# Optimization experiments

Measured on AMD Instinct MI355X. Metric: run time of the kernel, lower is better.

The kernel has to match this reference:

```python
import jax, jax.numpy as jnp
import numpy as np
from jax import lax


def _lstm_layer(x, h0, c0, W_ih, W_hh, b_ih, b_hh):
    # x: [B,T,I]; precompute input projection for all timesteps: [B,T,4H]
    xg = jnp.einsum('bti,gi->btg', x, W_ih) + b_ih

    def step(carry, xg_t):
        h, c = carry
        gates = xg_t + h @ W_hh.T + b_hh  # [B,4H]
        i, f, g, o = jnp.split(gates, 4, axis=-1)  # PyTorch LSTMCell gate order
        i = jax.nn.sigmoid(i)
        f = jax.nn.sigmoid(f)
        g = jnp.tanh(g)
        o = jax.nn.sigmoid(o)
        c = f * c + i * g
        h = o * jnp.tanh(c)
        return (h, c), h

    (h, c), ys = lax.scan(step, (h0, c0), jnp.swapaxes(xg, 0, 1))  # scan over T
    return jnp.swapaxes(ys, 0, 1), h, c  # [B,T,H], [B,H], [B,H]


def setup_inputs() -> dict:
    key = jax.random.key(0)
    ks = jax.random.split(key, 10)
    B, T, I, H = 128, 256, 256, 1024
    s = 0.02
    return {
        'x': jax.random.normal(ks[0], (B, T, I), jnp.float32),
        'hx0': jnp.zeros((2, B, H), jnp.float32),
        'cx0': jnp.zeros((2, B, H), jnp.float32),
        'W_ih0': jax.random.normal(ks[1], (4 * H, I), jnp.float32) * s,
        'W_hh0': jax.random.normal(ks[2], (4 * H, H), jnp.float32) * s,
        'b_ih0': jax.random.normal(ks[3], (4 * H,), jnp.float32) * s,
        'b_hh0': jax.random.normal(ks[4], (4 * H,), jnp.float32) * s,
        'W_ih1': jax.random.normal(ks[5], (4 * H, H), jnp.float32) * s,
        'W_hh1': jax.random.normal(ks[6], (4 * H, H), jnp.float32) * s,
        'b_ih1': jax.random.normal(ks[7], (4 * H,), jnp.float32) * s,
        'b_hh1': jax.random.normal(ks[8], (4 * H,), jnp.float32) * s,
    }


def reference(x, hx0, cx0, W_ih0, W_hh0, b_ih0, b_hh0, W_ih1, W_hh1, b_ih1, b_hh1):
    # Eval mode / variational_inference=False with dropout=0.0: masks are exact ones.
    x, h, c = _lstm_layer(x, hx0[0], cx0[0], W_ih0, W_hh0, b_ih0, b_hh0)
    x, h, c = _lstm_layer(x, hx0[1], cx0[1], W_ih1, W_hh1, b_ih1, b_hh1)
    return x, h, c
```

## Files before the change

### kernel.cpp

```cpp
#include <hip/hip_runtime.h>

typedef __attribute__((ext_vector_type(8))) short short8;
typedef __attribute__((ext_vector_type(4))) float f32x4;

#define DEV static __device__ __forceinline__

DEV unsigned short f2b(float f) {
    union { float f; unsigned u; } v; v.f = f;
    unsigned r = (v.u + 0x7FFFu + ((v.u >> 16) & 1u)) >> 16;
    return (unsigned short)r;
}
DEV float b2f(unsigned short s) {
    union { unsigned u; float f; } v; v.u = ((unsigned)s) << 16;
    return v.f;
}
DEV float sigm(float x) { return 1.0f / (1.0f + __expf(-x)); }


__global__ void k_f2b(const float* __restrict__ src, unsigned short* __restrict__ dst, int n4) {
    int i = blockIdx.x * blockDim.x + threadIdx.x;
    if (i < n4) {
        float4 v = ((const float4*)src)[i];
        ushort4 o;
        o.x = f2b(v.x); o.y = f2b(v.y); o.z = f2b(v.z); o.w = f2b(v.w);
        ((ushort4*)dst)[i] = o;
    }
}

__global__ void k_perm(const float* __restrict__ src, unsigned short* __restrict__ dst, int Kq) {
    int i = blockIdx.x * blockDim.x + threadIdx.x;
    int total = 4096 * Kq;
    if (i >= total) return;
    int rp = i / Kq, kq = i - rp * Kq;
    int j = rp >> 2, g = rp & 3;
    float4 v = ((const float4*)src)[(size_t)(g * 1024 + j) * Kq + kq];
    ushort4 o;
    o.x = f2b(v.x); o.y = f2b(v.y); o.z = f2b(v.z); o.w = f2b(v.w);
    ((ushort4*)dst)[(size_t)rp * Kq + kq] = o;
}

__global__ void k_bias(const float* __restrict__ bi0, const float* __restrict__ bh0,
                       const float* __restrict__ bi1, const float* __restrict__ bh1,
                       float* __restrict__ d0, float* __restrict__ d1) {
    int i = blockIdx.x * blockDim.x + threadIdx.x;
    if (i < 4096) {
        int j = i >> 2, g = i & 3, s = g * 1024 + j;
        d0[i] = bi0[s] + bh0[s];
        d1[i] = bi1[s] + bh1[s];
    }
}

__global__ void k_init(const float* __restrict__ hx, const float* __restrict__ cx,
                       unsigned* __restrict__ hB0, unsigned* __restrict__ hB1,
                       float* __restrict__ c0, float* __restrict__ c1) {
    int i = blockIdx.x * blockDim.x + threadIdx.x;
    if (i < 128 * 512) {
        int b = i >> 9, j = i & 511;
        const float* p0 = hx + (size_t)b * 1024 + j * 2;
        const float* p1 = hx + 131072 + (size_t)b * 1024 + j * 2;
        hB0[i] = (unsigned)f2b(p0[0]) | ((unsigned)f2b(p0[1]) << 16);
        hB1[i] = (unsigned)f2b(p1[0]) | ((unsigned)f2b(p1[1]) << 16);
        c0[i * 2] = cx[i * 2];
        c0[i * 2 + 1] = cx[i * 2 + 1];
        c1[i * 2] = cx[131072 + i * 2];
        c1[i * 2 + 1] = cx[131072 + i * 2 + 1];
    }
}

__global__ __launch_bounds__(256) void k_gemm(
    const unsigned short* __restrict__ A, const unsigned short* __restrict__ W,
    unsigned short* __restrict__ out, int K, int t0, int TC) {
    __shared__ unsigned short ldsA[128 * 40];
    __shared__ unsigned short ldsB[128 * 40];
    const int tid = threadIdx.x;
    const int w = tid >> 6, l = tid & 63;
    const int wm = w >> 1, wn = w & 1;
    const int bm = blockIdx.x, bn = blockIdx.y;
    const int lr = l & 15, lk = (l >> 4) * 8;

    const int row0 = tid >> 2, inb = (tid & 3) << 4;
    const int row1 = row0 + 64;
    const int v0 = bm * 128 + row0, v1 = bm * 128 + row1;
    const size_t ar0 = (size_t)((v0 / TC) * 256 + t0 + (v0 % TC));
    const size_t ar1 = (size_t)((v1 / TC) * 256 + t0 + (v1 % TC));
    const size_t br0 = (size_t)(bn * 128 + row0);
    const size_t br1 = (size_t)(bn * 128 + row1);

    f32x4 acc[4][4];
#pragma unroll
    for (int a = 0; a < 4; a++)
#pragma unroll
        for (int b = 0; b < 4; b++) acc[a][b] = (f32x4){0.f, 0.f, 0.f, 0.f};

    for (int ks = 0; ks < K; ks += 32) {
        uint4 a0 = *(const uint4*)((const char*)A + (ar0 * K + ks) * 2 + inb);
        uint4 a1 = *(const uint4*)((const char*)A + (ar1 * K + ks) * 2 + inb);
        uint4 b0 = *(const uint4*)((const char*)W + (br0 * K + ks) * 2 + inb);
        uint4 b1 = *(const uint4*)((const char*)W + (br1 * K + ks) * 2 + inb);
        *(uint4*)((char*)ldsA + row0 * 80 + inb) = a0;
        *(uint4*)((char*)ldsA + row1 * 80 + inb) = a1;
        *(uint4*)((char*)ldsB + row0 * 80 + inb) = b0;
        *(uint4*)((char*)ldsB + row1 * 80 + inb) = b1;
        __syncthreads();
        short8 af[4], bf[4];
#pragma unroll
        for (int mt = 0; mt < 4; mt++)
            af[mt] = *(const short8*)((const char*)ldsA + (wm * 64 + mt * 16 + lr) * 80 + lk * 2);
#pragma unroll
        for (int nt = 0; nt < 4; nt++)
            bf[nt] = *(const short8*)((const char*)ldsB + (wn * 64 + nt * 16 + lr) * 80 + lk * 2);
#pragma unroll
        for (int mt = 0; mt < 4; mt++)
#pragma unroll
            for (int nt = 0; nt < 4; nt++)
                acc[mt][nt] = __builtin_amdgcn_mfma_f32_16x16x32_bf16(af[mt], bf[nt], acc[mt][nt], 0, 0, 0);
        __syncthreads();
    }

#pragma unroll
    for (int mt = 0; mt < 4; mt++)
#pragma unroll
        for (int nt = 0; nt < 4; nt++)
#pragma unroll
            for (int v4 = 0; v4 < 4; v4++) {
                int vr = bm * 128 + wm * 64 + mt * 16 + (l >> 4) * 4 + v4;
                int col = bn * 128 + wn * 64 + nt * 16 + lr;
                out[(size_t)vr * 4096 + col] = f2b(acc[mt][nt][v4]);
            }
}

template<int LAYER>
__global__ __launch_bounds__(256, 1) void k_lstm(
    const unsigned short* __restrict__ Wh,
    const unsigned short* __restrict__ xg,
    const float* __restrict__ bias,
    float* __restrict__ cbuf,
    unsigned* __restrict__ hA,
    unsigned* __restrict__ hB,
    unsigned short* __restrict__ y0,
    float* __restrict__ out,
    unsigned* __restrict__ cnt,
    int t0, int TC)
{
    extern __shared__ char smem[];
    unsigned short* ldsW = (unsigned short*)smem;
    float* ldsP0 = (float*)(smem + 64 * 2064);
    float* ldsP1 = ldsP0 + 16 * 132;

    const int tid = threadIdx.x;
    const int g  = (int)blockIdx.x >> 5;
    const int nb = (int)blockIdx.x & 31;
    const int kq = tid >> 6;
    const int l  = tid & 63;
    const int lr = l & 15, lq = l >> 4;

    {
        const char* src = (const char*)(Wh + (size_t)nb * 128 * 1024);
#pragma unroll
        for (int it = 0; it < 32; it++) {
            int idx = it * 256 + tid;
            int row = idx >> 7, inr = (idx & 127) << 4;
            *(uint4*)(smem + row * 2064 + inr) = *(const uint4*)(src + (size_t)row * 2048 + inr);
        }
    }
    short8 wreg[32];
    {
        const unsigned short* src = Wh + (size_t)(nb * 128 + 64) * 1024 + kq * 256;
#pragma unroll
        for (int ct = 0; ct < 4; ct++)
#pragma unroll
            for (int kk = 0; kk < 8; kk++)
                wreg[ct * 8 + kk] =
                    *(const short8*)(src + (size_t)(ct * 16 + lr) * 1024 + kk * 32 + lq * 8);
    }

    const int er = tid >> 4, ep = tid & 15;
    const int eb = g * 16 + er;
    const int ec0 = nb * 128 + ep * 8;
    const int eu0 = nb * 32 + ep * 2;
    float2 c2 = *(const float2*)(cbuf + (size_t)eb * 1024 + eu0);
    const float4 bsA = *(const float4*)(bias + ec0);
    const float4 bsB = *(const float4*)(bias + ec0 + 4);

    const size_t abase = (size_t)(g * 16 + lr) * 256 + (size_t)kq * 64 + lq * 2;
    const char* wp = (const char*)ldsW + (size_t)lr * 2064 + kq * 512 + lq * 16;

    unsigned* cmy = cnt + g * 32;

    __syncthreads();

    for (int dt = 0; dt < TC; dt++) {
        const int t = t0 + dt;
        uint4 xv = *(const uint4*)(xg + (size_t)eb * ((size_t)TC * 4096) + (size_t)dt * 4096 + ec0);

        if (dt > 0) {
            unsigned tgt = 32u * (unsigned)dt;
            while (__hip_atomic_load(cmy, __ATOMIC_RELAXED, __HIP_MEMORY_SCOPE_AGENT) < tgt) {}
        }

        const unsigned long long* ap =
            (const unsigned long long*)((t & 1) ? hA : hB) + abase;
        f32x4 acc[8];
#pragma unroll
        for (int i = 0; i < 8; i++) acc[i] = (f32x4){0.f, 0.f, 0.f, 0.f};
#pragma unroll
        for (int kk = 0; kk < 8; kk++) {
            union { unsigned long long u[2]; short8 s; } av;
            av.u[0] = __hip_atomic_load(ap + kk * 8,     __ATOMIC_RELAXED, __HIP_MEMORY_SCOPE_AGENT);
            av.u[1] = __hip_atomic_load(ap + kk * 8 + 1, __ATOMIC_RELAXED, __HIP_MEMORY_SCOPE_AGENT);
#pragma unroll
            for (int ct = 0; ct < 4; ct++) {
                short8 b = *(const short8*)(wp + (size_t)ct * 16 * 2064 + kk * 64);
                acc[ct] = __builtin_amdgcn_mfma_f32_16x16x32_bf16(av.s, b, acc[ct], 0, 0, 0);
            }
#pragma unroll
            for (int ct = 0; ct < 4; ct++)
                acc[4 + ct] = __builtin_amdgcn_mfma_f32_16x16x32_bf16(av.s, wreg[ct * 8 + kk], acc[4 + ct], 0, 0, 0);
        }

        if (kq >= 2) {
            float* P = (kq == 2) ? ldsP0 : ldsP1;
#pragma unroll
            for (int i = 0; i < 8; i++)
#pragma unroll
                for (int v = 0; v < 4; v++)
                    P[(lq * 4 + v) * 132 + i * 16 + lr] = acc[i][v];
        }
        __syncthreads();
        if (kq < 2) {
            float* P = (kq == 0) ? ldsP0 : ldsP1;
#pragma unroll
            for (int i = 0; i < 8; i++)
#pragma unroll
                for (int v = 0; v < 4; v++)
                    P[(lq * 4 + v) * 132 + i * 16 + lr] += acc[i][v];
        }
        __syncthreads();

        float h0v, h1v;
        {
            const float* pa = ldsP0 + er * 132 + ep * 8;
            const float* pb = ldsP1 + er * 132 + ep * 8;
            const unsigned short* xs = (const unsigned short*)&xv;
            float p0 = pa[0] + pb[0] + b2f(xs[0]) + bsA.x;
            float p1 = pa[1] + pb[1] + b2f(xs[1]) + bsA.y;
            float p2 = pa[2] + pb[2] + b2f(xs[2]) + bsA.z;
            float p3 = pa[3] + pb[3] + b2f(xs[3]) + bsA.w;
            float q0 = pa[4] + pb[4] + b2f(xs[4]) + bsB.x;
            float q1 = pa[5] + pb[5] + b2f(xs[5]) + bsB.y;
            float q2 = pa[6] + pb[6] + b2f(xs[6]) + bsB.z;
            float q3 = pa[7] + pb[7] + b2f(xs[7]) + bsB.w;
            float i0 = sigm(p0), f0 = sigm(p1), gv0 = tanhf(p2), o0 = sigm(p3);
            float i1 = sigm(q0), f1 = sigm(q1), gv1 = tanhf(q2), o1 = sigm(q3);
            c2.x = f0 * c2.x + i0 * gv0;
            c2.y = f1 * c2.y + i1 * gv1;
            h0v = o0 * tanhf(c2.x);
            h1v = o1 * tanhf(c2.y);
            unsigned hp = (unsigned)f2b(h0v) | ((unsigned)f2b(h1v) << 16);
            unsigned* hout = (t & 1) ? hB : hA;
            __hip_atomic_store(hout + (size_t)eb * 512 + eu0 / 2, hp,
                               __ATOMIC_RELAXED, __HIP_MEMORY_SCOPE_AGENT);
        }
        __syncthreads();
        if (tid == 0)
            __hip_atomic_fetch_add(cmy, 1u, __ATOMIC_RELAXED, __HIP_MEMORY_SCOPE_AGENT);

        if (LAYER == 0) {
            unsigned hp = (unsigned)f2b(h0v) | ((unsigned)f2b(h1v) << 16);
            ((unsigned*)y0)[((size_t)eb * 256 + t) * 512 + eu0 / 2] = hp;
        } else {
            *(float2*)(out + ((size_t)eb * 256 + t) * 1024 + eu0) = make_float2(h0v, h1v);
            if (t == 255) {
                *(float2*)(out + (size_t)128 * 256 * 1024 + (size_t)eb * 1024 + eu0) =
                    make_float2(h0v, h1v);
                *(float2*)(out + (size_t)128 * 256 * 1024 + (size_t)128 * 1024 + (size_t)eb * 1024 + eu0) =
                    make_float2(c2.x, c2.y);
            }
        }
    }
    *(float2*)(cbuf + (size_t)eb * 1024 + eu0) = c2;
}


extern "C" void kernel_launch(void* const* d_in, const int* in_sizes, int n_in,
                              void* d_out, int out_size, void* d_ws, size_t ws_size,
                              hipStream_t stream) {
    const float* x    = (const float*)d_in[0];
    const float* hx0  = (const float*)d_in[1];
    const float* cx0  = (const float*)d_in[2];
    const float* Wih0 = (const float*)d_in[3];
    const float* Whh0 = (const float*)d_in[4];
    const float* bih0 = (const float*)d_in[5];
    const float* bhh0 = (const float*)d_in[6];
    const float* Wih1 = (const float*)d_in[7];
    const float* Whh1 = (const float*)d_in[8];
    const float* bih1 = (const float*)d_in[9];
    const float* bhh1 = (const float*)d_in[10];
    float* out = (float*)d_out;

    const int B = 128, T = 256, I = 256, H = 1024, G4 = 4096;
    const unsigned SMEM_BYTES = 64 * 2064 + 2 * 16 * 132 * 4;

    hipFuncSetAttribute((const void*)&k_lstm<0>, hipFuncAttributeMaxDynamicSharedMemorySize, SMEM_BYTES);
    hipFuncSetAttribute((const void*)&k_lstm<1>, hipFuncAttributeMaxDynamicSharedMemorySize, SMEM_BYTES);

    char* p = (char*)d_ws;
    auto alloc = [&](size_t bytes) { char* r = p; p += (bytes + 255) & ~(size_t)255; return r; };
    unsigned short* xbf   = (unsigned short*)alloc((size_t)B * T * I * 2);
    unsigned short* Wih0p = (unsigned short*)alloc((size_t)G4 * I * 2);
    unsigned short* Whh0p = (unsigned short*)alloc((size_t)G4 * H * 2);
    unsigned short* Wih1p = (unsigned short*)alloc((size_t)G4 * H * 2);
    unsigned short* Whh1p = (unsigned short*)alloc((size_t)G4 * H * 2);
    float* bias0 = (float*)alloc(G4 * 4);
    float* bias1 = (float*)alloc(G4 * 4);
    unsigned short* y0 = (unsigned short*)alloc((size_t)B * T * H * 2);
    unsigned* hA0 = (unsigned*)alloc((size_t)B * 512 * 4);
    unsigned* hB0 = (unsigned*)alloc((size_t)B * 512 * 4);
    unsigned* hA1 = (unsigned*)alloc((size_t)B * 512 * 4);
    unsigned* hB1 = (unsigned*)alloc((size_t)B * 512 * 4);
    float* c0 = (float*)alloc((size_t)B * H * 4);
    float* c1 = (float*)alloc((size_t)B * H * 4);
    unsigned* cnt = (unsigned*)alloc(8 * 128);
    size_t fixed = (size_t)(p - (char*)d_ws);
    int TC = 256;
    while (TC > 1 && fixed + (size_t)B * TC * G4 * 2 + 256 > ws_size) TC >>= 1;
    unsigned short* xg = (unsigned short*)alloc((size_t)B * TC * G4 * 2);

    k_f2b<<<(B * T * I / 4 + 255) / 256, 256, 0, stream>>>(x, xbf, B * T * I / 4);
    k_perm<<<(G4 * (I / 4) + 255) / 256, 256, 0, stream>>>(Wih0, Wih0p, I / 4);
    k_perm<<<(G4 * (H / 4) + 255) / 256, 256, 0, stream>>>(Whh0, Whh0p, H / 4);
    k_perm<<<(G4 * (H / 4) + 255) / 256, 256, 0, stream>>>(Wih1, Wih1p, H / 4);
    k_perm<<<(G4 * (H / 4) + 255) / 256, 256, 0, stream>>>(Whh1, Whh1p, H / 4);
    k_bias<<<16, 256, 0, stream>>>(bih0, bhh0, bih1, bhh1, bias0, bias1);
    k_init<<<256, 256, 0, stream>>>(hx0, cx0, hB0, hB1, c0, c1);

    for (int t0 = 0; t0 < T; t0 += TC) {
        k_gemm<<<dim3(TC, 32), 256, 0, stream>>>(xbf, Wih0p, xg, I, t0, TC);
        hipMemsetAsync(cnt, 0, 8 * 128, stream);
        int t0v = t0, TCv = TC;
        const unsigned short* Whp = Whh0p;
        const unsigned short* xgp = xg;
        const float* bp = bias0;
        float* cp = c0;
        unsigned* ha = hA0; unsigned* hb = hB0;
        unsigned short* y0p = y0;
        float* op = nullptr;
        unsigned* cp2 = cnt;
        void* args[] = {&Whp, &xgp, &bp, &cp, &ha, &hb, &y0p, &op, &cp2, &t0v, &TCv};
        hipLaunchCooperativeKernel((const void*)&k_lstm<0>, dim3(256), dim3(256), args, SMEM_BYTES, stream);
    }
    for (int t0 = 0; t0 < T; t0 += TC) {
        k_gemm<<<dim3(TC, 32), 256, 0, stream>>>(y0, Wih1p, xg, H, t0, TC);
        hipMemsetAsync(cnt, 0, 8 * 128, stream);
        int t0v = t0, TCv = TC;
        const unsigned short* Whp = Whh1p;
        const unsigned short* xgp = xg;
        const float* bp = bias1;
        float* cp = c1;
        unsigned* ha = hA1; unsigned* hb = hB1;
        unsigned short* y0p = nullptr;
        float* op = out;
        unsigned* cp2 = cnt;
        void* args[] = {&Whp, &xgp, &bp, &cp, &ha, &hb, &y0p, &op, &cp2, &t0v, &TCv};
        hipLaunchCooperativeKernel((const void*)&k_lstm<1>, dim3(256), dim3(256), args, SMEM_BYTES, stream);
    }
}
```

Baseline: 3.118 ms.

## Replace per-group atomic counter barrier with per-block step flags and partial waits

Each block now publishes its completed timestep in its own padded flag slot with a plain atomic store, in place of a fetch_add on a shared counter. Each wavefront polls only the 8 producer blocks whose hidden-state slice feeds its K quarter, so it no longer waits for all 32 blocks in the group. This is meant to remove atomic contention on one cache line and let wavefronts start their MFMA work earlier. Flags hold absolute timesteps, so they are cleared once per launch rather than memset before every chunk, at the cost of 8 polled loads per spin iteration.

```diff
diff --git a/kernel.cpp b/kernel.cpp
--- a/kernel.cpp
+++ b/kernel.cpp
@@ -139,7 +139,7 @@
     unsigned* __restrict__ hB,
     unsigned short* __restrict__ y0,
     float* __restrict__ out,
-    unsigned* __restrict__ cnt,
+    unsigned* __restrict__ flags,
     int t0, int TC)
 {
     extern __shared__ char smem[];
@@ -185,7 +185,8 @@
     const size_t abase = (size_t)(g * 16 + lr) * 256 + (size_t)kq * 64 + lq * 2;
     const char* wp = (const char*)ldsW + (size_t)lr * 2064 + kq * 512 + lq * 16;
 
-    unsigned* cmy = cnt + g * 32;
+    const unsigned* fpoll = flags + (size_t)(g * 32 + kq * 8) * 16;
+    unsigned* fmine = flags + (size_t)(g * 32 + nb) * 16;
 
     __syncthreads();
 
@@ -193,9 +194,16 @@
         const int t = t0 + dt;
         uint4 xv = *(const uint4*)(xg + (size_t)eb * ((size_t)TC * 4096) + (size_t)dt * 4096 + ec0);
 
-        if (dt > 0) {
-            unsigned tgt = 32u * (unsigned)dt;
-            while (__hip_atomic_load(cmy, __ATOMIC_RELAXED, __HIP_MEMORY_SCOPE_AGENT) < tgt) {}
+        if (t > 0) {
+            const unsigned tgt = (unsigned)t;
+            for (;;) {
+                unsigned ok = 1;
+#pragma unroll
+                for (int j = 0; j < 8; j++)
+                    ok &= (__hip_atomic_load(fpoll + j * 16, __ATOMIC_RELAXED,
+                                             __HIP_MEMORY_SCOPE_AGENT) >= tgt) ? 1u : 0u;
+                if (ok) break;
+            }
         }
 
         const unsigned long long* ap =
@@ -263,7 +271,8 @@
         }
         __syncthreads();
         if (tid == 0)
-            __hip_atomic_fetch_add(cmy, 1u, __ATOMIC_RELAXED, __HIP_MEMORY_SCOPE_AGENT);
+            __hip_atomic_store(fmine, (unsigned)(t + 1),
+                               __ATOMIC_RELAXED, __HIP_MEMORY_SCOPE_AGENT);
 
         if (LAYER == 0) {
             unsigned hp = (unsigned)f2b(h0v) | ((unsigned)f2b(h1v) << 16);
@@ -300,6 +309,7 @@
 
     const int B = 128, T = 256, I = 256, H = 1024, G4 = 4096;
     const unsigned SMEM_BYTES = 64 * 2064 + 2 * 16 * 132 * 4;
+    const int FLAGS_U32 = 8 * 32 * 16;
 
     hipFuncSetAttribute((const void*)&k_lstm<0>, hipFuncAttributeMaxDynamicSharedMemorySize, SMEM_BYTES);
     hipFuncSetAttribute((const void*)&k_lstm<1>, hipFuncAttributeMaxDynamicSharedMemorySize, SMEM_BYTES);
@@ -320,12 +330,14 @@
     unsigned* hB1 = (unsigned*)alloc((size_t)B * 512 * 4);
     float* c0 = (float*)alloc((size_t)B * H * 4);
     float* c1 = (float*)alloc((size_t)B * H * 4);
-    unsigned* cnt = (unsigned*)alloc(8 * 128);
+    unsigned* flags0 = (unsigned*)alloc((size_t)2 * FLAGS_U32 * 4);
+    unsigned* flags1 = flags0 + FLAGS_U32;
     size_t fixed = (size_t)(p - (char*)d_ws);
     int TC = 256;
     while (TC > 1 && fixed + (size_t)B * TC * G4 * 2 + 256 > ws_size) TC >>= 1;
     unsigned short* xg = (unsigned short*)alloc((size_t)B * TC * G4 * 2);
 
+    hipMemsetAsync(flags0, 0, (size_t)2 * FLAGS_U32 * 4, stream);
     k_f2b<<<(B * T * I / 4 + 255) / 256, 256, 0, stream>>>(x, xbf, B * T * I / 4);
     k_perm<<<(G4 * (I / 4) + 255) / 256, 256, 0, stream>>>(Wih0, Wih0p, I / 4);
     k_perm<<<(G4 * (H / 4) + 255) / 256, 256, 0, stream>>>(Whh0, Whh0p, H / 4);
@@ -336,7 +348,6 @@
 
     for (int t0 = 0; t0 < T; t0 += TC) {
         k_gemm<<<dim3(TC, 32), 256, 0, stream>>>(xbf, Wih0p, xg, I, t0, TC);
-        hipMemsetAsync(cnt, 0, 8 * 128, stream);
         int t0v = t0, TCv = TC;
         const unsigned short* Whp = Whh0p;
         const unsigned short* xgp = xg;
@@ -345,13 +356,12 @@
         unsigned* ha = hA0; unsigned* hb = hB0;
         unsigned short* y0p = y0;
         float* op = nullptr;
-        unsigned* cp2 = cnt;
-        void* args[] = {&Whp, &xgp, &bp, &cp, &ha, &hb, &y0p, &op, &cp2, &t0v, &TCv};
+        unsigned* fl = flags0;
+        void* args[] = {&Whp, &xgp, &bp, &cp, &ha, &hb, &y0p, &op, &fl, &t0v, &TCv};
         hipLaunchCooperativeKernel((const void*)&k_lstm<0>, dim3(256), dim3(256), args, SMEM_BYTES, stream);
     }
     for (int t0 = 0; t0 < T; t0 += TC) {
         k_gemm<<<dim3(TC, 32), 256, 0, stream>>>(y0, Wih1p, xg, H, t0, TC);
-        hipMemsetAsync(cnt, 0, 8 * 128, stream);
         int t0v = t0, TCv = TC;
         const unsigned short* Whp = Whh1p;
         const unsigned short* xgp = xg;
@@ -360,8 +370,8 @@
         unsigned* ha = hA1; unsigned* hb = hB1;
         unsigned short* y0p = nullptr;
         float* op = out;
-        unsigned* cp2 = cnt;
-        void* args[] = {&Whp, &xgp, &bp, &cp, &ha, &hb, &y0p, &op, &cp2, &t0v, &TCv};
+        unsigned* fl = flags1;
+        void* args[] = {&Whp, &xgp, &bp, &cp, &ha, &hb, &y0p, &op, &fl, &t0v, &TCv};
         hipLaunchCooperativeKernel((const void*)&k_lstm<1>, dim3(256), dim3(256), args, SMEM_BYTES, stream);
     }
 }
```

Result: slower. 3.234 ms (+3.7%).

## Split LSTM recurrent K-reduction across eight waves per block

Applied to the files above, without the earlier changes.

Doubles the recurrent kernel's block from 256 to 512 threads, so each of eight waves covers a 128-wide K slice instead of four waves covering 256. The per-wave MFMA chain per step and the register-resident weight slice are both halved. Partial sums are reduced through three LDS buffers over an extra barrier stage, and only the first 256 threads run the gate math. The aim is lower per-step latency on the sequential critical path, paid for with an additional __syncthreads and more LDS traffic per timestep.

```diff
diff --git a/kernel.cpp b/kernel.cpp
--- a/kernel.cpp
+++ b/kernel.cpp
@@ -130,7 +130,7 @@
 }
 
 template<int LAYER>
-__global__ __launch_bounds__(256, 1) void k_lstm(
+__global__ __launch_bounds__(512, 2) void k_lstm(
     const unsigned short* __restrict__ Wh,
     const unsigned short* __restrict__ xg,
     const float* __restrict__ bias,
@@ -144,46 +144,52 @@
 {
     extern __shared__ char smem[];
     unsigned short* ldsW = (unsigned short*)smem;
-    float* ldsP0 = (float*)(smem + 64 * 2064);
-    float* ldsP1 = ldsP0 + 16 * 132;
+    float* P0 = (float*)(smem + 64 * 2064);
+    float* P1 = P0 + 16 * 132;
+    float* P2 = P1 + 16 * 132;
 
     const int tid = threadIdx.x;
     const int g  = (int)blockIdx.x >> 5;
     const int nb = (int)blockIdx.x & 31;
-    const int kq = tid >> 6;
+    const int w  = tid >> 6;
     const int l  = tid & 63;
     const int lr = l & 15, lq = l >> 4;
 
     {
         const char* src = (const char*)(Wh + (size_t)nb * 128 * 1024);
 #pragma unroll
-        for (int it = 0; it < 32; it++) {
-            int idx = it * 256 + tid;
+        for (int it = 0; it < 16; it++) {
+            int idx = it * 512 + tid;
             int row = idx >> 7, inr = (idx & 127) << 4;
             *(uint4*)(smem + row * 2064 + inr) = *(const uint4*)(src + (size_t)row * 2048 + inr);
         }
     }
-    short8 wreg[32];
+    short8 wreg[16];
     {
-        const unsigned short* src = Wh + (size_t)(nb * 128 + 64) * 1024 + kq * 256;
+        const unsigned short* src = Wh + (size_t)(nb * 128 + 64) * 1024 + w * 128;
 #pragma unroll
         for (int ct = 0; ct < 4; ct++)
 #pragma unroll
-            for (int kk = 0; kk < 8; kk++)
-                wreg[ct * 8 + kk] =
+            for (int kk = 0; kk < 4; kk++)
+                wreg[ct * 4 + kk] =
                     *(const short8*)(src + (size_t)(ct * 16 + lr) * 1024 + kk * 32 + lq * 8);
     }
 
     const int er = tid >> 4, ep = tid & 15;
-    const int eb = g * 16 + er;
+    const int eb = g * 16 + (er & 15);
     const int ec0 = nb * 128 + ep * 8;
     const int eu0 = nb * 32 + ep * 2;
-    float2 c2 = *(const float2*)(cbuf + (size_t)eb * 1024 + eu0);
-    const float4 bsA = *(const float4*)(bias + ec0);
-    const float4 bsB = *(const float4*)(bias + ec0 + 4);
-
-    const size_t abase = (size_t)(g * 16 + lr) * 256 + (size_t)kq * 64 + lq * 2;
-    const char* wp = (const char*)ldsW + (size_t)lr * 2064 + kq * 512 + lq * 16;
+    float2 c2 = make_float2(0.f, 0.f);
+    float4 bsA = make_float4(0.f, 0.f, 0.f, 0.f);
+    float4 bsB = make_float4(0.f, 0.f, 0.f, 0.f);
+    if (tid < 256) {
+        c2 = *(const float2*)(cbuf + (size_t)eb * 1024 + eu0);
+        bsA = *(const float4*)(bias + ec0);
+        bsB = *(const float4*)(bias + ec0 + 4);
+    }
+
+    const size_t abase = (size_t)(g * 16 + lr) * 256 + (size_t)w * 32 + lq * 2;
+    const char* wp = (const char*)ldsW + (size_t)lr * 2064 + w * 256 + lq * 16;
 
     unsigned* cmy = cnt + g * 32;
 
@@ -191,7 +197,9 @@
 
     for (int dt = 0; dt < TC; dt++) {
         const int t = t0 + dt;
-        uint4 xv = *(const uint4*)(xg + (size_t)eb * ((size_t)TC * 4096) + (size_t)dt * 4096 + ec0);
+        uint4 xv = make_uint4(0, 0, 0, 0);
+        if (tid < 256)
+            xv = *(const uint4*)(xg + (size_t)eb * ((size_t)TC * 4096) + (size_t)dt * 4096 + ec0);
 
         if (dt > 0) {
             unsigned tgt = 32u * (unsigned)dt;
@@ -204,7 +212,7 @@
 #pragma unroll
         for (int i = 0; i < 8; i++) acc[i] = (f32x4){0.f, 0.f, 0.f, 0.f};
 #pragma unroll
-        for (int kk = 0; kk < 8; kk++) {
+        for (int kk = 0; kk < 4; kk++) {
             union { unsigned long long u[2]; short8 s; } av;
             av.u[0] = __hip_atomic_load(ap + kk * 8,     __ATOMIC_RELAXED, __HIP_MEMORY_SCOPE_AGENT);
             av.u[1] = __hip_atomic_load(ap + kk * 8 + 1, __ATOMIC_RELAXED, __HIP_MEMORY_SCOPE_AGENT);
@@ -215,11 +223,11 @@
             }
 #pragma unroll
             for (int ct = 0; ct < 4; ct++)
-                acc[4 + ct] = __builtin_amdgcn_mfma_f32_16x16x32_bf16(av.s, wreg[ct * 8 + kk], acc[4 + ct], 0, 0, 0);
-        }
-
-        if (kq >= 2) {
-            float* P = (kq == 2) ? ldsP0 : ldsP1;
+                acc[4 + ct] = __builtin_amdgcn_mfma_f32_16x16x32_bf16(av.s, wreg[ct * 4 + kk], acc[4 + ct], 0, 0, 0);
+        }
+
+        if (w >= 5) {
+            float* P = (w == 5) ? P0 : (w == 6) ? P1 : P2;
 #pragma unroll
             for (int i = 0; i < 8; i++)
 #pragma unroll
@@ -227,8 +235,8 @@
                     P[(lq * 4 + v) * 132 + i * 16 + lr] = acc[i][v];
         }
         __syncthreads();
-        if (kq < 2) {
-            float* P = (kq == 0) ? ldsP0 : ldsP1;
+        if (w >= 2 && w <= 4) {
+            float* P = (w == 2) ? P0 : (w == 3) ? P1 : P2;
 #pragma unroll
             for (int i = 0; i < 8; i++)
 #pragma unroll
@@ -236,20 +244,30 @@
                     P[(lq * 4 + v) * 132 + i * 16 + lr] += acc[i][v];
         }
         __syncthreads();
-
-        float h0v, h1v;
-        {
-            const float* pa = ldsP0 + er * 132 + ep * 8;
-            const float* pb = ldsP1 + er * 132 + ep * 8;
+        if (w < 2) {
+            float* P = (w == 0) ? P0 : P1;
+#pragma unroll
+            for (int i = 0; i < 8; i++)
+#pragma unroll
+                for (int v = 0; v < 4; v++)
+                    P[(lq * 4 + v) * 132 + i * 16 + lr] += acc[i][v];
+        }
+        __syncthreads();
+
+        float h0v = 0.f, h1v = 0.f;
+        if (tid < 256) {
+            const float* pa = P0 + er * 132 + ep * 8;
+            const float* pb = P1 + er * 132 + ep * 8;
+            const float* pc = P2 + er * 132 + ep * 8;
             const unsigned short* xs = (const unsigned short*)&xv;
-            float p0 = pa[0] + pb[0] + b2f(xs[0]) + bsA.x;
-            float p1 = pa[1] + pb[1] + b2f(xs[1]) + bsA.y;
-            float p2 = pa[2] + pb[2] + b2f(xs[2]) + bsA.z;
-            float p3 = pa[3] + pb[3] + b2f(xs[3]) + bsA.w;
-            float q0 = pa[4] + pb[4] + b2f(xs[4]) + bsB.x;
-            float q1 = pa[5] + pb[5] + b2f(xs[5]) + bsB.y;
-            float q2 = pa[6] + pb[6] + b2f(xs[6]) + bsB.z;
-            float q3 = pa[7] + pb[7] + b2f(xs[7]) + bsB.w;
+            float p0 = pa[0] + pb[0] + pc[0] + b2f(xs[0]) + bsA.x;
+            float p1 = pa[1] + pb[1] + pc[1] + b2f(xs[1]) + bsA.y;
+            float p2 = pa[2] + pb[2] + pc[2] + b2f(xs[2]) + bsA.z;
+            float p3 = pa[3] + pb[3] + pc[3] + b2f(xs[3]) + bsA.w;
+            float q0 = pa[4] + pb[4] + pc[4] + b2f(xs[4]) + bsB.x;
+            float q1 = pa[5] + pb[5] + pc[5] + b2f(xs[5]) + bsB.y;
+            float q2 = pa[6] + pb[6] + pc[6] + b2f(xs[6]) + bsB.z;
+            float q3 = pa[7] + pb[7] + pc[7] + b2f(xs[7]) + bsB.w;
             float i0 = sigm(p0), f0 = sigm(p1), gv0 = tanhf(p2), o0 = sigm(p3);
             float i1 = sigm(q0), f1 = sigm(q1), gv1 = tanhf(q2), o1 = sigm(q3);
             c2.x = f0 * c2.x + i0 * gv0;
@@ -265,20 +283,23 @@
         if (tid == 0)
             __hip_atomic_fetch_add(cmy, 1u, __ATOMIC_RELAXED, __HIP_MEMORY_SCOPE_AGENT);
 
-        if (LAYER == 0) {
-            unsigned hp = (unsigned)f2b(h0v) | ((unsigned)f2b(h1v) << 16);
-            ((unsigned*)y0)[((size_t)eb * 256 + t) * 512 + eu0 / 2] = hp;
-        } else {
-            *(float2*)(out + ((size_t)eb * 256 + t) * 1024 + eu0) = make_float2(h0v, h1v);
-            if (t == 255) {
-                *(float2*)(out + (size_t)128 * 256 * 1024 + (size_t)eb * 1024 + eu0) =
-                    make_float2(h0v, h1v);
-                *(float2*)(out + (size_t)128 * 256 * 1024 + (size_t)128 * 1024 + (size_t)eb * 1024 + eu0) =
-                    make_float2(c2.x, c2.y);
+        if (tid < 256) {
+            if (LAYER == 0) {
+                unsigned hp = (unsigned)f2b(h0v) | ((unsigned)f2b(h1v) << 16);
+                ((unsigned*)y0)[((size_t)eb * 256 + t) * 512 + eu0 / 2] = hp;
+            } else {
+                *(float2*)(out + ((size_t)eb * 256 + t) * 1024 + eu0) = make_float2(h0v, h1v);
+                if (t == 255) {
+                    *(float2*)(out + (size_t)128 * 256 * 1024 + (size_t)eb * 1024 + eu0) =
+                        make_float2(h0v, h1v);
+                    *(float2*)(out + (size_t)128 * 256 * 1024 + (size_t)128 * 1024 + (size_t)eb * 1024 + eu0) =
+                        make_float2(c2.x, c2.y);
+                }
             }
         }
     }
-    *(float2*)(cbuf + (size_t)eb * 1024 + eu0) = c2;
+    if (tid < 256)
+        *(float2*)(cbuf + (size_t)eb * 1024 + eu0) = c2;
 }
 
 
@@ -299,7 +320,7 @@
     float* out = (float*)d_out;
 
     const int B = 128, T = 256, I = 256, H = 1024, G4 = 4096;
-    const unsigned SMEM_BYTES = 64 * 2064 + 2 * 16 * 132 * 4;
+    const unsigned SMEM_BYTES = 64 * 2064 + 3 * 16 * 132 * 4;
 
     hipFuncSetAttribute((const void*)&k_lstm<0>, hipFuncAttributeMaxDynamicSharedMemorySize, SMEM_BYTES);
     hipFuncSetAttribute((const void*)&k_lstm<1>, hipFuncAttributeMaxDynamicSharedMemorySize, SMEM_BYTES);
@@ -347,7 +368,7 @@
         float* op = nullptr;
         unsigned* cp2 = cnt;
         void* args[] = {&Whp, &xgp, &bp, &cp, &ha, &hb, &y0p, &op, &cp2, &t0v, &TCv};
-        hipLaunchCooperativeKernel((const void*)&k_lstm<0>, dim3(256), dim3(256), args, SMEM_BYTES, stream);
+        hipLaunchCooperativeKernel((const void*)&k_lstm<0>, dim3(256), dim3(512), args, SMEM_BYTES, stream);
     }
     for (int t0 = 0; t0 < T; t0 += TC) {
         k_gemm<<<dim3(TC, 32), 256, 0, stream>>>(y0, Wih1p, xg, H, t0, TC);
@@ -362,6 +383,6 @@
         float* op = out;
         unsigned* cp2 = cnt;
         void* args[] = {&Whp, &xgp, &bp, &cp, &ha, &hb, &y0p, &op, &cp2, &t0v, &TCv};
-        hipLaunchCooperativeKernel((const void*)&k_lstm<1>, dim3(256), dim3(256), args, SMEM_BYTES, stream);
-    }
-}
+        hipLaunchCooperativeKernel((const void*)&k_lstm<1>, dim3(256), dim3(512), args, SMEM_BYTES, stream);
+    }
+}
```

Result: no change. 3.091 ms (-0.9%).
